# Optimization experiments

Hardware: AMD Instinct MI355X
Metric: run time of the kernel (lower is better)

The kernel has to match this reference:

```python
import jax, jax.numpy as jnp
import numpy as np

N, E, D = 50000, 800000, 256

def setup_inputs() -> dict:
    key = jax.random.key(0)
    ks = jax.random.split(key, 12)
    s = 1.0 / np.sqrt(D)
    return {
        "x": jax.random.normal(ks[0], (N, D), dtype=jnp.float32),
        "src": jax.random.randint(ks[1], (E,), 0, N, dtype=jnp.int64),
        "dst": jax.random.randint(ks[2], (E,), 0, N, dtype=jnp.int64),
        "W_w": jax.random.normal(ks[3], (D, D), dtype=jnp.float32) * s,
        "W_b": jnp.zeros((D,), dtype=jnp.float32),
        "U_w": jax.random.normal(ks[4], (D, D), dtype=jnp.float32) * s,
        "U_b": jnp.zeros((D,), dtype=jnp.float32),
        "V_w": jax.random.normal(ks[5], (D, D), dtype=jnp.float32) * s,
        "V_b": jnp.zeros((D,), dtype=jnp.float32),
        "attn_l": jax.random.normal(ks[6], (D,), dtype=jnp.float32) * s,
        "attn_r": jax.random.normal(ks[7], (D,), dtype=jnp.float32) * s,
        "gamma": jnp.ones((D,), dtype=jnp.float32),
        "beta": jnp.zeros((D,), dtype=jnp.float32),
    }

def reference(x, src, dst, W_w, W_b, U_w, U_b, V_w, V_b, attn_l, attn_r, gamma, beta):
    # node transforms (dropout p=0 -> identity)
    Wh = x @ W_w + W_b            # [N, D]
    Uh = x @ U_w + U_b            # [N, D]
    Vh = x @ V_w + V_b            # [N, D]
    out_src = Wh * attn_l         # [N, D]
    out_dst = Wh * attn_r         # [N, D]
    # per-edge gate: sigma = sigmoid(out_src[u] + out_dst[v])  [E, D]
    sigma = jax.nn.sigmoid(out_src[src] + out_dst[dst])
    # aggregate to destination nodes
    sum_sigma_h = jax.ops.segment_sum(Vh[src] * sigma, dst, num_segments=N)
    sum_sigma = jax.ops.segment_sum(sigma, dst, num_segments=N)
    h = Uh + sum_sigma_h / (sum_sigma + 1e-6)
    # layer norm (eps=1e-6, affine)
    mu = jnp.mean(h, axis=-1, keepdims=True)
    var = jnp.mean((h - mu) ** 2, axis=-1, keepdims=True)
    h = (h - mu) / jnp.sqrt(var + 1e-6) * gamma + beta
    h = jax.nn.relu(h)
    return x + h  # residual
```

## Files before the change

### kernel.cpp

```cpp
#include <hip/hip_runtime.h>
#include <hip/hip_bf16.h>

#define NN 50000
#define NE 800000
#define NB 196
#define NROWPAD 50048

#define XCVT_BLOCKS 6250
#define TW_BLOCKS   192
#define HIST_BLOCKS 3125
#define SCAT_BLOCKS 3125
#define GEMM_BLOCKS (391*3)

typedef __attribute__((ext_vector_type(8))) short short8;
typedef __attribute__((ext_vector_type(4))) float floatx4;
typedef unsigned short u16;
typedef unsigned int u32;

__device__ __forceinline__ u16 f2bf(float f) {
    u32 u = __float_as_uint(f);
    u += 0x7FFFu + ((u >> 16) & 1u);
    return (u16)(u >> 16);
}
__device__ __forceinline__ float bf_lo(u32 u) { return __uint_as_float(u << 16); }
__device__ __forceinline__ float bf_hi(u32 u) { return __uint_as_float(u & 0xFFFF0000u); }
__device__ __forceinline__ u32 pack_bf(float lo, float hi) {
    return (u32)f2bf(lo) | ((u32)f2bf(hi) << 16);
}
__device__ __forceinline__ void gl_lds16(const void* g, void* l) {
    __builtin_amdgcn_global_load_lds((const __attribute__((address_space(1))) void*)g,
                                     (__attribute__((address_space(3))) void*)l, 16, 0, 0);
}

#if __has_builtin(__builtin_amdgcn_exp2f)
#define EXP2F(x) __builtin_amdgcn_exp2f(x)
#else
#define EXP2F(x) exp2f(x)
#endif

__global__ __launch_bounds__(256) void prep_kernel(
    const float* __restrict__ x, u16* __restrict__ xbf,
    const float* __restrict__ W, const float* __restrict__ U, const float* __restrict__ V,
    u16* __restrict__ wT, const int* __restrict__ dst, int* __restrict__ deg) {
    __shared__ float s[32][33];
    int b = blockIdx.x;
    if (b < XCVT_BLOCKS) {
        size_t i = ((size_t)b * 256 + threadIdx.x) * 8;
        floatx4 f0 = *(const floatx4*)(x + i);
        floatx4 f1 = *(const floatx4*)(x + i + 4);
        uint4 pk;
        pk.x = pack_bf(f0[0], f0[1]);
        pk.y = pack_bf(f0[2], f0[3]);
        pk.z = pack_bf(f1[0], f1[1]);
        pk.w = pack_bf(f1[2], f1[3]);
        *(uint4*)(xbf + i) = pk;
    } else if (b < XCVT_BLOCKS + TW_BLOCKS) {
        int bb = b - XCVT_BLOCKS;
        int g = bb >> 6, rem = bb & 63;
        int r0 = (rem & 7) * 32, c0 = (rem >> 3) * 32;
        const float* M = (g == 0) ? W : ((g == 1) ? U : V);
        int tx = threadIdx.x & 31, ty = threadIdx.x >> 5;
#pragma unroll
        for (int k = 0; k < 4; ++k)
            s[ty + k * 8][tx] = M[(size_t)(r0 + ty + k * 8) * 256 + c0 + tx];
        __syncthreads();
#pragma unroll
        for (int k = 0; k < 4; ++k)
            wT[(size_t)(g * 256 + c0 + ty + k * 8) * 256 + r0 + tx] = f2bf(s[tx][ty + k * 8]);
    } else {
        int e = (b - XCVT_BLOCKS - TW_BLOCKS) * 256 + threadIdx.x;
        if (e < NE) atomicAdd(&deg[dst[e]], 1);
    }
}

__global__ __launch_bounds__(256) void scanA_kernel(const int* __restrict__ deg, int* __restrict__ bsum) {
    int t = threadIdx.x;
    int i = blockIdx.x * 256 + t;
    int v = (i < NN) ? deg[i] : 0;
#pragma unroll
    for (int m = 32; m; m >>= 1) v += __shfl_xor(v, m, 64);
    __shared__ int ws[4];
    if ((t & 63) == 0) ws[t >> 6] = v;
    __syncthreads();
    if (t == 0) bsum[blockIdx.x] = ws[0] + ws[1] + ws[2] + ws[3];
}

__global__ __launch_bounds__(256) void scanB_kernel(const int* __restrict__ bsum, int* __restrict__ bpre,
                                                    int* __restrict__ rows_end) {
    int t = threadIdx.x, lane = t & 63, wv = t >> 6;
    int v = (t < NB) ? bsum[t] : 0;
    int inc = v;
#pragma unroll
    for (int off = 1; off < 64; off <<= 1) {
        int u = __shfl_up(inc, off, 64);
        if (lane >= off) inc += u;
    }
    __shared__ int wsum[4];
    if (lane == 63) wsum[wv] = inc;
    __syncthreads();
    int woff = 0;
    for (int k = 0; k < wv; ++k) woff += wsum[k];
    if (t < NB) bpre[t] = woff + inc - v;
    if (t == 255) rows_end[0] = woff + inc;
}

__global__ __launch_bounds__(256) void scanC_kernel(const int* __restrict__ deg, const int* __restrict__ bpre,
                                                    int* __restrict__ rows, int* __restrict__ cursor) {
    int t = threadIdx.x, lane = t & 63, wv = t >> 6;
    int i = blockIdx.x * 256 + t;
    int v = (i < NN) ? deg[i] : 0;
    int inc = v;
#pragma unroll
    for (int off = 1; off < 64; off <<= 1) {
        int u = __shfl_up(inc, off, 64);
        if (lane >= off) inc += u;
    }
    __shared__ int wsum[4];
    if (lane == 63) wsum[wv] = inc;
    __syncthreads();
    int woff = bpre[blockIdx.x];
    for (int k = 0; k < wv; ++k) woff += wsum[k];
    int excl = woff + inc - v;
    if (i < NN) { rows[i] = excl; cursor[i] = excl; }
}

template<bool USE_BF>
__global__ __launch_bounds__(256, 2) void gemmsc_kernel(
    const u16* __restrict__ xbf, const float* __restrict__ xf, const u16* __restrict__ wT,
    const float* __restrict__ Wb, const float* __restrict__ Ub, const float* __restrict__ Vb,
    u16* __restrict__ WVh, float* __restrict__ Uh,
    const int* __restrict__ src, const int* __restrict__ dst,
    int* __restrict__ cursor, int* __restrict__ esrc) {
    __shared__ __align__(16) u16 As[128 * 64];
    __shared__ __align__(16) u16 Bs[2][128 * 64];

    int b = blockIdx.x;
    if (b < SCAT_BLOCKS) {
        int e = b * 256 + threadIdx.x;
        if (e < NE) {
            int d = dst[e];
            int pos = atomicAdd(&cursor[d], 1);
            esrc[pos] = src[e];
        }
        return;
    }
    int gb = b - SCAT_BLOCKS;
    int rb = (gb % 391) * 128;
    int cgy = gb / 391;
    int cbg = cgy * 256;

    int t = threadIdx.x, lane = t & 63, w = t >> 6;
    int wm = w >> 1, wn = w & 1;

    floatx4 acc[2][4][4] = {};

    int subrow = lane >> 3;
    int qv = lane & 7;
    int a_row = t >> 1;
    int a_half = t & 1;

    for (int kt = 0; kt < 4; ++kt) {
        int k0 = kt * 64;
#pragma unroll
        for (int ii = 0; ii < 4; ++ii) {
            int rowbase = (w * 4 + ii) * 8;
            int row = rowbase + subrow;
            int qa = qv ^ (row & 7);
            gl_lds16(wT + (size_t)(cbg + row) * 256 + k0 + qa * 8, Bs[0] + rowbase * 64);
            gl_lds16(wT + (size_t)(cbg + 128 + row) * 256 + k0 + qa * 8, Bs[1] + rowbase * 64);
            if (USE_BF)
                gl_lds16(xbf + (size_t)(rb + row) * 256 + k0 + qa * 8, As + rowbase * 64);
        }
        if (!USE_BF) {
            int grow = rb + a_row;
            uint4 pk[4] = {};
            if (grow < NN) {
                const float* px = xf + (size_t)grow * 256 + k0 + a_half * 32;
#pragma unroll
                for (int c = 0; c < 4; ++c) {
                    floatx4 f0 = *(const floatx4*)(px + c * 8);
                    floatx4 f1 = *(const floatx4*)(px + c * 8 + 4);
                    pk[c].x = pack_bf(f0[0], f0[1]);
                    pk[c].y = pack_bf(f0[2], f0[3]);
                    pk[c].z = pack_bf(f1[0], f1[1]);
                    pk[c].w = pack_bf(f1[2], f1[3]);
                }
            }
#pragma unroll
            for (int c = 0; c < 4; ++c) {
                int q = a_half * 4 + c;
                *(uint4*)(As + a_row * 64 + ((q ^ (a_row & 7)) * 8)) = pk[c];
            }
        }
        __syncthreads();

#pragma unroll
        for (int s = 0; s < 2; ++s) {
            short8 a[4], bfr[2][4];
            int q = s * 4 + (lane >> 4);
#pragma unroll
            for (int i = 0; i < 4; ++i) {
                int ar = wm * 64 + i * 16 + (lane & 15);
                a[i] = *(const short8*)(As + ar * 64 + ((q ^ (ar & 7)) * 8));
            }
#pragma unroll
            for (int ch = 0; ch < 2; ++ch)
#pragma unroll
                for (int j = 0; j < 4; ++j) {
                    int br = wn * 64 + j * 16 + (lane & 15);
                    bfr[ch][j] = *(const short8*)(Bs[ch] + br * 64 + ((q ^ (br & 7)) * 8));
                }
#pragma unroll
            for (int ch = 0; ch < 2; ++ch)
#pragma unroll
                for (int i = 0; i < 4; ++i)
#pragma unroll
                    for (int j = 0; j < 4; ++j)
                        acc[ch][i][j] = __builtin_amdgcn_mfma_f32_16x16x32_bf16(
                            a[i], bfr[ch][j], acc[ch][i][j], 0, 0, 0);
        }
        __syncthreads();
    }

    const float* bias = (cgy == 0) ? Wb : ((cgy == 1) ? Ub : Vb);
#pragma unroll
    for (int ch = 0; ch < 2; ++ch)
#pragma unroll
        for (int i = 0; i < 4; ++i)
#pragma unroll
            for (int j = 0; j < 4; ++j) {
                int col = ch * 128 + wn * 64 + j * 16 + (lane & 15);
                float bv = bias[col];
#pragma unroll
                for (int r = 0; r < 4; ++r) {
                    int row = rb + wm * 64 + i * 16 + (lane >> 4) * 4 + r;
                    if (row < NN) {
                        float val = acc[ch][i][j][r] + bv;
                        if (cgy == 0)      WVh[(size_t)row * 512 + col] = f2bf(val);
                        else if (cgy == 1) Uh[(size_t)row * 256 + col] = val;
                        else               WVh[(size_t)row * 512 + 256 + col] = f2bf(val);
                    }
                }
            }
}

__global__ __launch_bounds__(256) void node_kernel(
    const u16* __restrict__ WVh, const float* __restrict__ x,
    const int* __restrict__ rows, const int* __restrict__ esrc,
    const float* __restrict__ attn_l, const float* __restrict__ attn_r,
    const float* __restrict__ gamma, const float* __restrict__ beta,
    float* inout) {
    int wv = threadIdx.x >> 6, lane = threadIdx.x & 63;
    int v = blockIdx.x * 4 + wv;
    if (v >= NN) return;
    int c0 = lane * 4;

    const float NL2E = -1.44269504f;
    floatx4 alv = *(const floatx4*)(attn_l + c0);
    floatx4 arv = *(const floatx4*)(attn_r + c0);
    uint2 wvv = *(const uint2*)(WVh + (size_t)v * 512 + c0);
    float al2[4] = { alv[0] * NL2E, alv[1] * NL2E, alv[2] * NL2E, alv[3] * NL2E };
    float td2[4] = { bf_lo(wvv.x) * arv[0] * NL2E, bf_hi(wvv.x) * arv[1] * NL2E,
                     bf_lo(wvv.y) * arv[2] * NL2E, bf_hi(wvv.y) * arv[3] * NL2E };

    float acc_h[4] = {0.f, 0.f, 0.f, 0.f};
    float acc_s[4] = {0.f, 0.f, 0.f, 0.f};

    auto edge = [&](uint2 wu, uint2 vu) {
        float wf[4] = { bf_lo(wu.x), bf_hi(wu.x), bf_lo(wu.y), bf_hi(wu.y) };
        float vf[4] = { bf_lo(vu.x), bf_hi(vu.x), bf_lo(vu.y), bf_hi(vu.y) };
#pragma unroll
        for (int j = 0; j < 4; ++j) {
            float m = fmaf(wf[j], al2[j], td2[j]);
            float s = __builtin_amdgcn_rcpf(1.0f + EXP2F(m));
            acc_s[j] += s;
            acc_h[j] = fmaf(s, vf[j], acc_h[j]);
        }
    };

    int e = rows[v], e1 = rows[v + 1];
    for (; e + 8 <= e1; e += 8) {
        int us[8];
#pragma unroll
        for (int q = 0; q < 8; ++q) us[q] = esrc[e + q];
        uint2 wu[8], vu[8];
#pragma unroll
        for (int q = 0; q < 8; ++q) {
            const u16* p = WVh + (size_t)us[q] * 512 + c0;
            wu[q] = *(const uint2*)p;
            vu[q] = *(const uint2*)(p + 256);
        }
#pragma unroll
        for (int q = 0; q < 8; ++q) edge(wu[q], vu[q]);
    }
    for (; e + 2 <= e1; e += 2) {
        int ua = esrc[e], ub = esrc[e + 1];
        const u16* pa = WVh + (size_t)ua * 512 + c0;
        const u16* pb = WVh + (size_t)ub * 512 + c0;
        uint2 wa = *(const uint2*)pa, va = *(const uint2*)(pa + 256);
        uint2 wb = *(const uint2*)pb, vb = *(const uint2*)(pb + 256);
        edge(wa, va); edge(wb, vb);
    }
    for (; e < e1; ++e) {
        int u = esrc[e];
        const u16* p = WVh + (size_t)u * 512 + c0;
        uint2 wu = *(const uint2*)p, vu = *(const uint2*)(p + 256);
        edge(wu, vu);
    }

    floatx4 uh = *(const floatx4*)(inout + (size_t)v * 256 + c0);
    float h[4];
#pragma unroll
    for (int j = 0; j < 4; ++j)
        h[j] = uh[j] + acc_h[j] * __builtin_amdgcn_rcpf(acc_s[j] + 1e-6f);

    float s01 = h[0] + h[1] + h[2] + h[3];
#pragma unroll
    for (int m = 32; m; m >>= 1) s01 += __shfl_xor(s01, m, 64);
    float mu = s01 * (1.0f / 256.0f);
    float d[4] = { h[0] - mu, h[1] - mu, h[2] - mu, h[3] - mu };
    float sq = d[0] * d[0] + d[1] * d[1] + d[2] * d[2] + d[3] * d[3];
#pragma unroll
    for (int m = 32; m; m >>= 1) sq += __shfl_xor(sq, m, 64);
    float inv = rsqrtf(sq * (1.0f / 256.0f) + 1e-6f);

    floatx4 gm = *(const floatx4*)(gamma + c0);
    floatx4 bt = *(const floatx4*)(beta + c0);
    floatx4 xr = *(const floatx4*)(x + (size_t)v * 256 + c0);
    floatx4 res;
#pragma unroll
    for (int j = 0; j < 4; ++j) {
        float y = d[j] * inv * gm[j] + bt[j];
        y = fmaxf(y, 0.0f);
        res[j] = xr[j] + y;
    }
    *(floatx4*)(inout + (size_t)v * 256 + c0) = res;
}

extern "C" void kernel_launch(void* const* d_in, const int* in_sizes, int n_in,
                              void* d_out, int out_size, void* d_ws, size_t ws_size,
                              hipStream_t stream) {
    const float* x       = (const float*)d_in[0];
    const int*   src     = (const int*)d_in[1];
    const int*   dst     = (const int*)d_in[2];
    const float* W_w     = (const float*)d_in[3];
    const float* W_b     = (const float*)d_in[4];
    const float* U_w     = (const float*)d_in[5];
    const float* U_b     = (const float*)d_in[6];
    const float* V_w     = (const float*)d_in[7];
    const float* V_b     = (const float*)d_in[8];
    const float* attn_l  = (const float*)d_in[9];
    const float* attn_r  = (const float*)d_in[10];
    const float* gamma   = (const float*)d_in[11];
    const float* beta    = (const float*)d_in[12];

    char* ws = (char*)d_ws;
    size_t off = 0;
    auto alloc = [&](size_t bytes) -> char* {
        char* p = ws + off;
        off += (bytes + 255) & ~(size_t)255;
        return p;
    };
    u16* WVh     = (u16*)alloc((size_t)NN * 512 * 2);
    u16* wT      = (u16*)alloc((size_t)768 * 256 * 2);
    int* deg     = (int*)alloc((size_t)NN * 4);
    int* rows    = (int*)alloc((size_t)(NN + 1) * 4);
    int* cursor  = (int*)alloc((size_t)NN * 4);
    int* esrc    = (int*)alloc((size_t)NE * 4);
    int* bsum    = (int*)alloc((size_t)NB * 4);
    int* bpre    = (int*)alloc((size_t)NB * 4);
    u16* xbf     = (u16*)alloc((size_t)NROWPAD * 256 * 2);
    bool use_bf  = (ws_size >= off);

    float* Uh_f32 = (float*)d_out;

    hipMemsetAsync(deg, 0, (size_t)NN * 4, stream);

    if (use_bf) {
        prep_kernel<<<XCVT_BLOCKS + TW_BLOCKS + HIST_BLOCKS, 256, 0, stream>>>(
            x, xbf, W_w, U_w, V_w, wT, dst, deg);
    } else {
        prep_kernel<<<XCVT_BLOCKS + TW_BLOCKS + HIST_BLOCKS, 256, 0, stream>>>(
            x, (u16*)wT , W_w, U_w, V_w, wT, dst, deg);
    }

    scanA_kernel<<<NB, 256, 0, stream>>>(deg, bsum);
    scanB_kernel<<<1, 256, 0, stream>>>(bsum, bpre, rows + NN);
    scanC_kernel<<<NB, 256, 0, stream>>>(deg, bpre, rows, cursor);

    int gs_blocks = SCAT_BLOCKS + GEMM_BLOCKS;
    if (use_bf) {
        gemmsc_kernel<true><<<gs_blocks, 256, 0, stream>>>(
            xbf, x, wT, W_b, U_b, V_b, WVh, Uh_f32, src, dst, cursor, esrc);
    } else {
        gemmsc_kernel<false><<<gs_blocks, 256, 0, stream>>>(
            nullptr, x, wT, W_b, U_b, V_b, WVh, Uh_f32, src, dst, cursor, esrc);
    }

    node_kernel<<<(NN + 3) / 4, 256, 0, stream>>>(
        WVh, x, rows, esrc, attn_l, attn_r, gamma, beta, (float*)d_out);
}
```

Before: 295.4 us.

## Restructure GEMM to keep A fragments in registers and split scatter kernel

Replaces the fused scatter+GEMM kernel with a separate scatter kernel and a new GEMM. In the new GEMM each block loads a full 128x256 slice of the transposed weights into LDS once and keeps its A rows in registers across the whole K dimension, using a 2D grid of 128-column groups. The loop has a single barrier, whereas the old one staged A and B in K-tiles of 64 with two barriers each. The prep kernel also skips the x conversion blocks when the bf16 buffer is unused. The cost is 64 KB of LDS per block and large register pressure from 16 A fragments, which could reduce occupancy. The scatter's atomics no longer overlap with GEMM work, and A rows are now re-read for each of the six column groups.

```diff
diff --git a/kernel.cpp b/kernel.cpp
--- a/kernel.cpp
+++ b/kernel.cpp
@@ -9,8 +9,6 @@
 #define XCVT_BLOCKS 6250
 #define TW_BLOCKS   192
 #define HIST_BLOCKS 3125
-#define SCAT_BLOCKS 3125
-#define GEMM_BLOCKS (391*3)
 
 typedef __attribute__((ext_vector_type(8))) short short8;
 typedef __attribute__((ext_vector_type(4))) float floatx4;
@@ -41,10 +39,11 @@
 __global__ __launch_bounds__(256) void prep_kernel(
     const float* __restrict__ x, u16* __restrict__ xbf,
     const float* __restrict__ W, const float* __restrict__ U, const float* __restrict__ V,
-    u16* __restrict__ wT, const int* __restrict__ dst, int* __restrict__ deg) {
+    u16* __restrict__ wT, const int* __restrict__ dst, int* __restrict__ deg, int do_xcvt) {
     __shared__ float s[32][33];
     int b = blockIdx.x;
-    if (b < XCVT_BLOCKS) {
+    int xb = do_xcvt ? XCVT_BLOCKS : 0;
+    if (b < xb) {
         size_t i = ((size_t)b * 256 + threadIdx.x) * 8;
         floatx4 f0 = *(const floatx4*)(x + i);
         floatx4 f1 = *(const floatx4*)(x + i + 4);
@@ -54,8 +53,8 @@
         pk.z = pack_bf(f1[0], f1[1]);
         pk.w = pack_bf(f1[2], f1[3]);
         *(uint4*)(xbf + i) = pk;
-    } else if (b < XCVT_BLOCKS + TW_BLOCKS) {
-        int bb = b - XCVT_BLOCKS;
+    } else if (b < xb + TW_BLOCKS) {
+        int bb = b - xb;
         int g = bb >> 6, rem = bb & 63;
         int r0 = (rem & 7) * 32, c0 = (rem >> 3) * 32;
         const float* M = (g == 0) ? W : ((g == 1) ? U : V);
@@ -68,7 +67,7 @@
         for (int k = 0; k < 4; ++k)
             wT[(size_t)(g * 256 + c0 + ty + k * 8) * 256 + r0 + tx] = f2bf(s[tx][ty + k * 8]);
     } else {
-        int e = (b - XCVT_BLOCKS - TW_BLOCKS) * 256 + threadIdx.x;
+        int e = (b - xb - TW_BLOCKS) * 256 + threadIdx.x;
         if (e < NE) atomicAdd(&deg[dst[e]], 1);
     }
 }
@@ -124,124 +123,95 @@
     if (i < NN) { rows[i] = excl; cursor[i] = excl; }
 }
 
+__global__ void scatter_kernel(const int* __restrict__ src, const int* __restrict__ dst,
+                               int* __restrict__ cursor, int* __restrict__ esrc) {
+    int e = blockIdx.x * 256 + threadIdx.x;
+    if (e < NE) {
+        int d = dst[e];
+        int pos = atomicAdd(&cursor[d], 1);
+        esrc[pos] = src[e];
+    }
+}
+
 template<bool USE_BF>
-__global__ __launch_bounds__(256, 2) void gemmsc_kernel(
+__global__ __launch_bounds__(256, 2) void gemm2_kernel(
     const u16* __restrict__ xbf, const float* __restrict__ xf, const u16* __restrict__ wT,
     const float* __restrict__ Wb, const float* __restrict__ Ub, const float* __restrict__ Vb,
-    u16* __restrict__ WVh, float* __restrict__ Uh,
-    const int* __restrict__ src, const int* __restrict__ dst,
-    int* __restrict__ cursor, int* __restrict__ esrc) {
-    __shared__ __align__(16) u16 As[128 * 64];
-    __shared__ __align__(16) u16 Bs[2][128 * 64];
-
-    int b = blockIdx.x;
-    if (b < SCAT_BLOCKS) {
-        int e = b * 256 + threadIdx.x;
-        if (e < NE) {
-            int d = dst[e];
-            int pos = atomicAdd(&cursor[d], 1);
-            esrc[pos] = src[e];
+    u16* __restrict__ WVh, float* __restrict__ Uh) {
+    __shared__ __align__(16) u16 Bs[128 * 256];
+
+    int rb = blockIdx.x * 128;
+    int cgy = blockIdx.y;
+    int cbg = cgy * 128;
+    int t = threadIdx.x, lane = t & 63, w = t >> 6;
+
+    int arow = rb + w * 32 + (lane & 15);
+    short8 afr[2][8];
+    if (USE_BF) {
+#pragma unroll
+        for (int rg = 0; rg < 2; ++rg)
+#pragma unroll
+            for (int ks = 0; ks < 8; ++ks)
+                afr[rg][ks] = *(const short8*)(xbf + (size_t)(arow + rg * 16) * 256 + ks * 32 + (lane >> 4) * 8);
+    } else {
+#pragma unroll
+        for (int rg = 0; rg < 2; ++rg)
+#pragma unroll
+            for (int ks = 0; ks < 8; ++ks) {
+                int row = arow + rg * 16;
+                const float* p = xf + ((size_t)(row < NN ? row : 0)) * 256 + ks * 32 + (lane >> 4) * 8;
+                floatx4 f0 = *(const floatx4*)(p);
+                floatx4 f1 = *(const floatx4*)(p + 4);
+                uint4 pk;
+                pk.x = pack_bf(f0[0], f0[1]);
+                pk.y = pack_bf(f0[2], f0[3]);
+                pk.z = pack_bf(f1[0], f1[1]);
+                pk.w = pack_bf(f1[2], f1[3]);
+                afr[rg][ks] = *(short8*)&pk;
+            }
+    }
+
+#pragma unroll
+    for (int i = 0; i < 16; ++i) {
+        int ci = (w * 16 + i) * 2 + (lane >> 5);
+        int q = (lane & 31) ^ (ci & 7);
+        gl_lds16(wT + (size_t)(cbg + ci) * 256 + q * 8, Bs + (w * 16 + i) * 512);
+    }
+    __syncthreads();
+
+    floatx4 acc[2][8] = {};
+#pragma unroll
+    for (int ks = 0; ks < 8; ++ks) {
+#pragma unroll
+        for (int cf = 0; cf < 8; ++cf) {
+            int ci = cf * 16 + (lane & 15);
+            int q = (ks * 4 + (lane >> 4)) ^ (ci & 7);
+            short8 bfrag = *(const short8*)(Bs + ci * 256 + q * 8);
+            acc[0][cf] = __builtin_amdgcn_mfma_f32_16x16x32_bf16(afr[0][ks], bfrag, acc[0][cf], 0, 0, 0);
+            acc[1][cf] = __builtin_amdgcn_mfma_f32_16x16x32_bf16(afr[1][ks], bfrag, acc[1][cf], 0, 0, 0);
         }
-        return;
-    }
-    int gb = b - SCAT_BLOCKS;
-    int rb = (gb % 391) * 128;
-    int cgy = gb / 391;
-    int cbg = cgy * 256;
-
-    int t = threadIdx.x, lane = t & 63, w = t >> 6;
-    int wm = w >> 1, wn = w & 1;
-
-    floatx4 acc[2][4][4] = {};
-
-    int subrow = lane >> 3;
-    int qv = lane & 7;
-    int a_row = t >> 1;
-    int a_half = t & 1;
-
-    for (int kt = 0; kt < 4; ++kt) {
-        int k0 = kt * 64;
-#pragma unroll
-        for (int ii = 0; ii < 4; ++ii) {
-            int rowbase = (w * 4 + ii) * 8;
-            int row = rowbase + subrow;
-            int qa = qv ^ (row & 7);
-            gl_lds16(wT + (size_t)(cbg + row) * 256 + k0 + qa * 8, Bs[0] + rowbase * 64);
-            gl_lds16(wT + (size_t)(cbg + 128 + row) * 256 + k0 + qa * 8, Bs[1] + rowbase * 64);
-            if (USE_BF)
-                gl_lds16(xbf + (size_t)(rb + row) * 256 + k0 + qa * 8, As + rowbase * 64);
-        }
-        if (!USE_BF) {
-            int grow = rb + a_row;
-            uint4 pk[4] = {};
-            if (grow < NN) {
-                const float* px = xf + (size_t)grow * 256 + k0 + a_half * 32;
-#pragma unroll
-                for (int c = 0; c < 4; ++c) {
-                    floatx4 f0 = *(const floatx4*)(px + c * 8);
-                    floatx4 f1 = *(const floatx4*)(px + c * 8 + 4);
-                    pk[c].x = pack_bf(f0[0], f0[1]);
-                    pk[c].y = pack_bf(f0[2], f0[3]);
-                    pk[c].z = pack_bf(f1[0], f1[1]);
-                    pk[c].w = pack_bf(f1[2], f1[3]);
+    }
+
+    int g = cbg >> 8;
+    int cloc = cbg & 255;
+    const float* bias = (g == 0) ? Wb : ((g == 1) ? Ub : Vb);
+#pragma unroll
+    for (int rg = 0; rg < 2; ++rg)
+#pragma unroll
+        for (int cf = 0; cf < 8; ++cf) {
+            int col = cloc + cf * 16 + (lane & 15);
+            float bv = bias[col];
+#pragma unroll
+            for (int r = 0; r < 4; ++r) {
+                int row = rb + w * 32 + rg * 16 + (lane >> 4) * 4 + r;
+                if (row < NN) {
+                    float val = acc[rg][cf][r] + bv;
+                    if (g == 0)      WVh[(size_t)row * 512 + col] = f2bf(val);
+                    else if (g == 1) Uh[(size_t)row * 256 + col] = val;
+                    else             WVh[(size_t)row * 512 + 256 + col] = f2bf(val);
                 }
             }
-#pragma unroll
-            for (int c = 0; c < 4; ++c) {
-                int q = a_half * 4 + c;
-                *(uint4*)(As + a_row * 64 + ((q ^ (a_row & 7)) * 8)) = pk[c];
-            }
         }
-        __syncthreads();
-
-#pragma unroll
-        for (int s = 0; s < 2; ++s) {
-            short8 a[4], bfr[2][4];
-            int q = s * 4 + (lane >> 4);
-#pragma unroll
-            for (int i = 0; i < 4; ++i) {
-                int ar = wm * 64 + i * 16 + (lane & 15);
-                a[i] = *(const short8*)(As + ar * 64 + ((q ^ (ar & 7)) * 8));
-            }
-#pragma unroll
-            for (int ch = 0; ch < 2; ++ch)
-#pragma unroll
-                for (int j = 0; j < 4; ++j) {
-                    int br = wn * 64 + j * 16 + (lane & 15);
-                    bfr[ch][j] = *(const short8*)(Bs[ch] + br * 64 + ((q ^ (br & 7)) * 8));
-                }
-#pragma unroll
-            for (int ch = 0; ch < 2; ++ch)
-#pragma unroll
-                for (int i = 0; i < 4; ++i)
-#pragma unroll
-                    for (int j = 0; j < 4; ++j)
-                        acc[ch][i][j] = __builtin_amdgcn_mfma_f32_16x16x32_bf16(
-                            a[i], bfr[ch][j], acc[ch][i][j], 0, 0, 0);
-        }
-        __syncthreads();
-    }
-
-    const float* bias = (cgy == 0) ? Wb : ((cgy == 1) ? Ub : Vb);
-#pragma unroll
-    for (int ch = 0; ch < 2; ++ch)
-#pragma unroll
-        for (int i = 0; i < 4; ++i)
-#pragma unroll
-            for (int j = 0; j < 4; ++j) {
-                int col = ch * 128 + wn * 64 + j * 16 + (lane & 15);
-                float bv = bias[col];
-#pragma unroll
-                for (int r = 0; r < 4; ++r) {
-                    int row = rb + wm * 64 + i * 16 + (lane >> 4) * 4 + r;
-                    if (row < NN) {
-                        float val = acc[ch][i][j][r] + bv;
-                        if (cgy == 0)      WVh[(size_t)row * 512 + col] = f2bf(val);
-                        else if (cgy == 1) Uh[(size_t)row * 256 + col] = val;
-                        else               WVh[(size_t)row * 512 + 256 + col] = f2bf(val);
-                    }
-                }
-            }
 }
 
 __global__ __launch_bounds__(256) void node_kernel(
@@ -376,25 +346,20 @@
 
     hipMemsetAsync(deg, 0, (size_t)NN * 4, stream);
 
-    if (use_bf) {
-        prep_kernel<<<XCVT_BLOCKS + TW_BLOCKS + HIST_BLOCKS, 256, 0, stream>>>(
-            x, xbf, W_w, U_w, V_w, wT, dst, deg);
-    } else {
-        prep_kernel<<<XCVT_BLOCKS + TW_BLOCKS + HIST_BLOCKS, 256, 0, stream>>>(
-            x, (u16*)wT , W_w, U_w, V_w, wT, dst, deg);
-    }
+    int xb = use_bf ? XCVT_BLOCKS : 0;
+    prep_kernel<<<xb + TW_BLOCKS + HIST_BLOCKS, 256, 0, stream>>>(
+        x, xbf, W_w, U_w, V_w, wT, dst, deg, use_bf ? 1 : 0);
 
     scanA_kernel<<<NB, 256, 0, stream>>>(deg, bsum);
     scanB_kernel<<<1, 256, 0, stream>>>(bsum, bpre, rows + NN);
     scanC_kernel<<<NB, 256, 0, stream>>>(deg, bpre, rows, cursor);
-
-    int gs_blocks = SCAT_BLOCKS + GEMM_BLOCKS;
+    scatter_kernel<<<(NE + 255) / 256, 256, 0, stream>>>(src, dst, cursor, esrc);
+
+    dim3 gg((NN + 127) / 128, 6);
     if (use_bf) {
-        gemmsc_kernel<true><<<gs_blocks, 256, 0, stream>>>(
-            xbf, x, wT, W_b, U_b, V_b, WVh, Uh_f32, src, dst, cursor, esrc);
+        gemm2_kernel<true><<<gg, 256, 0, stream>>>(xbf, x, wT, W_b, U_b, V_b, WVh, Uh_f32);
     } else {
-        gemmsc_kernel<false><<<gs_blocks, 256, 0, stream>>>(
-            nullptr, x, wT, W_b, U_b, V_b, WVh, Uh_f32, src, dst, cursor, esrc);
+        gemm2_kernel<false><<<gg, 256, 0, stream>>>(nullptr, x, wT, W_b, U_b, V_b, WVh, Uh_f32);
     }
 
     node_kernel<<<(NN + 3) / 4, 256, 0, stream>>>(
```

Result: slower. 304.7 us (+3.1%).
